# Kernel tuning notes

Measured on AMD Instinct MI355X. Metric: run time of the kernel, lower is better.

## Reference

```python
import jax, jax.numpy as jnp
import numpy as np

# SSMBlock constants (from init_kwargs and standard mamba_ssm defaults)
W = 8            # pooled spatial edge; d_model = W^3
K = 16           # AvgPool3d kernel & stride
D_MODEL = W ** 3            # 512
D_STATE = 16
EXPAND = 2
D_INNER = EXPAND * D_MODEL  # 1024
DT_RANK = D_MODEL // 16     # 32 (ceil(512/16))
D_CONV = 4


def setup_inputs() -> dict:
    key = jax.random.key(0)
    ks = jax.random.split(key, 8)
    s = 0.02
    x = jax.random.normal(ks[0], (1, 64, 128, 128, 128), dtype=jnp.float32)
    in_proj_w = jax.random.normal(ks[1], (2 * D_INNER, D_MODEL), jnp.float32) * s
    conv_w = jax.random.normal(ks[2], (D_INNER, D_CONV), jnp.float32) * s
    conv_b = jnp.zeros((D_INNER,), jnp.float32)
    x_proj_w = jax.random.normal(ks[3], (DT_RANK + 2 * D_STATE, D_INNER), jnp.float32) * s
    dt_proj_w = jax.random.normal(ks[4], (D_INNER, DT_RANK), jnp.float32) * s
    dt_proj_b = jax.random.uniform(ks[5], (D_INNER,), jnp.float32, minval=-4.0, maxval=-2.0)
    A_log = jnp.log(jnp.broadcast_to(jnp.arange(1, D_STATE + 1, dtype=jnp.float32), (D_INNER, D_STATE)))
    D = jnp.ones((D_INNER,), jnp.float32)
    out_proj_w = jax.random.normal(ks[6], (D_MODEL, D_INNER), jnp.float32) * s
    return dict(x=x, in_proj_w=in_proj_w, conv_w=conv_w, conv_b=conv_b,
                x_proj_w=x_proj_w, dt_proj_w=dt_proj_w, dt_proj_b=dt_proj_b,
                A_log=A_log, D=D, out_proj_w=out_proj_w)


def _forward(x, in_proj_w, conv_w, conv_b, x_proj_w, dt_proj_w, dt_proj_b, A_log, D, out_proj_w):
    B, C = x.shape[0], x.shape[1]
    # AvgPool3d(K, stride=K): non-overlapping -> reshape + mean
    xp = x.reshape(B, C, W, K, W, K, W, K).mean(axis=(3, 5, 7))  # (B,C,W,W,W)
    seq = xp.reshape(B, C, D_MODEL)  # Mamba input: L = C, d_model = W^3

    # in_proj -> (x, z)
    xz = jnp.einsum('bld,ed->ble', seq, in_proj_w)  # (B,L,2*D_INNER)
    xs, z = jnp.split(xz, 2, axis=-1)

    # causal depthwise conv1d along L + SiLU
    xt = jnp.pad(xs, ((0, 0), (D_CONV - 1, 0), (0, 0))).transpose(0, 2, 1)  # (B,E,L+pad)
    conv = jax.lax.conv_general_dilated(
        xt, conv_w[:, None, :], window_strides=(1,), padding='VALID',
        dimension_numbers=('NCH', 'OIH', 'NCH'), feature_group_count=D_INNER)
    xs = jax.nn.silu(conv.transpose(0, 2, 1) + conv_b)  # (B,L,E)

    # input-dependent dt, B, C
    x_dbl = jnp.einsum('ble,fe->blf', xs, x_proj_w)
    dt, Bs, Cs = jnp.split(x_dbl, [DT_RANK, DT_RANK + D_STATE], axis=-1)
    dt = jax.nn.softplus(jnp.einsum('blr,er->ble', dt, dt_proj_w) + dt_proj_b)  # (B,L,E)

    # selective scan: h_t = exp(dt*A) h_{t-1} + (dt*x) B_t ; y_t = <h_t, C_t> + D*x_t
    A = -jnp.exp(A_log)                                  # (E,S)
    dA = jnp.exp(dt[..., None] * A)                      # (B,L,E,S)
    dBx = (dt * xs)[..., None] * Bs[:, :, None, :]       # (B,L,E,S)

    def step(h, inp):
        da, dbx, c = inp
        h = da * h + dbx                                 # (B,E,S)
        y = jnp.einsum('bes,bs->be', h, c)
        return h, y

    h0 = jnp.zeros((B, D_INNER, D_STATE), xs.dtype)
    _, ys = jax.lax.scan(step, h0, (dA.transpose(1, 0, 2, 3), dBx.transpose(1, 0, 2, 3), Cs.transpose(1, 0, 2)))
    y = ys.transpose(1, 0, 2) + xs * D                   # (B,L,E)

    y = y * jax.nn.silu(z)
    out = jnp.einsum('ble,de->bld', y, out_proj_w)       # (B,L,d_model)
    return out.reshape(B, C, W, W, W)


def reference(x, in_proj_w, conv_w, conv_b, x_proj_w, dt_proj_w, dt_proj_b, A_log, D, out_proj_w):
    return _forward(x, in_proj_w, conv_w, conv_b, x_proj_w, dt_proj_w, dt_proj_b, A_log, D, out_proj_w)
```

## Files before the change

### kernel.cpp

```cpp
#include <hip/hip_runtime.h>
#include <math.h>

typedef float f32x4 __attribute__((ext_vector_type(4)));

__device__ __forceinline__ float dot4v(f32x4 a, f32x4 b){
    return a.x*b.x + a.y*b.y + a.z*b.z + a.w*b.w;
}
__device__ __forceinline__ float dot4(float4 a, float4 b){
    return a.x*b.x + a.y*b.y + a.z*b.z + a.w*b.w;
}

__device__ __forceinline__ float reduce4(float a0, float a1, float a2, float a3, int lane){
    int b0 = lane & 1, b1 = lane & 2;
    float r  = b0 ? a1 : a0;
    float rt = b0 ? a0 : a1;
    r += __shfl_xor(rt, 1);
    float s  = b0 ? a3 : a2;
    float st = b0 ? a2 : a3;
    s += __shfl_xor(st, 1);
    float u  = b1 ? s : r;
    float ut = b1 ? r : s;
    u += __shfl_xor(ut, 2);
    u += __shfl_xor(u, 4);
    u += __shfl_xor(u, 8);
    u += __shfl_xor(u, 16);
    u += __shfl_xor(u, 32);
    return u;
}

__global__ __launch_bounds__(256) void pool_k(const float* __restrict__ x,
                                              float* __restrict__ seq){
    __shared__ float red[4][8];
    int tid  = threadIdx.x;
    int lane = tid & 63;
    int part = tid >> 6;
    int cdh  = blockIdx.x;
    int c  = cdh >> 6;
    int od = (cdh >> 3) & 7;
    int oh = cdh & 7;
    int half = lane >> 5;
    int f    = lane & 31;

    const f32x4* px = (const f32x4*)x;
    size_t base = ((size_t)(c * 128 + od * 16) * 128 + (size_t)(oh * 16 + half)) * 32 + f
                + (size_t)part * 4 * 4096;

    float acc = 0.f;
    #pragma unroll
    for (int ii = 0; ii < 4; ii++){
        size_t o = base + (size_t)ii * 4096;
        #pragma unroll
        for (int jj = 0; jj < 8; jj++){
            f32x4 v = __builtin_nontemporal_load(&px[o + (size_t)jj * 64]);
            acc += (v.x + v.y) + (v.z + v.w);
        }
    }
    acc += __shfl_xor(acc, 1);
    acc += __shfl_xor(acc, 2);
    acc += __shfl_xor(acc, 32);
    if (lane < 32 && (lane & 3) == 0) red[part][lane >> 2] = acc;
    __syncthreads();
    if (tid < 8){
        float v = red[0][tid] + red[1][tid] + red[2][tid] + red[3][tid];
        seq[c * 512 + od * 64 + oh * 8 + tid] = v * (1.0f / 4096.0f);
    }
}

__global__ __launch_bounds__(256) void inproj_k(const float* __restrict__ seq,
                                                const float* __restrict__ Win,
                                                float* __restrict__ xz){
    int lane = threadIdx.x & 63;
    int wid  = blockIdx.x * 4 + (threadIdx.x >> 6);
    int l0 = (wid >> 7) << 3;
    int e0 = (wid & 127) << 4;
    const f32x4* S = (const f32x4*)seq;
    f32x4 sa[8], sb[8];
    #pragma unroll
    for (int r = 0; r < 8; r++){
        sa[r] = S[(size_t)(l0 + r) * 128 + lane];
        sb[r] = S[(size_t)(l0 + r) * 128 + lane + 64];
    }
    #pragma unroll 2
    for (int j = 0; j < 16; j++){
        int e = e0 + j;
        const f32x4* W = (const f32x4*)Win + (size_t)e * 128;
        f32x4 w0 = W[lane], w1 = W[lane + 64];
        float a[8];
        #pragma unroll
        for (int r = 0; r < 8; r++) a[r] = dot4v(w0, sa[r]) + dot4v(w1, sb[r]);
        float u0 = reduce4(a[0], a[1], a[2], a[3], lane);
        float u1 = reduce4(a[4], a[5], a[6], a[7], lane);
        if (lane < 4){
            xz[(size_t)(l0 + lane) * 2048 + e]     = u0;
            xz[(size_t)(l0 + 4 + lane) * 2048 + e] = u1;
        }
    }
}

__global__ __launch_bounds__(256) void xpc_k(const float* __restrict__ xz,
                                             const float* __restrict__ cw,
                                             const float* __restrict__ cb,
                                             const float* __restrict__ Wx,
                                             float* __restrict__ xsT,
                                             float* __restrict__ zsT,
                                             float* __restrict__ bcT,
                                             float* __restrict__ xdT){
    __shared__ float xs_row[1024];
    int bid = blockIdx.x;
    int l  = bid >> 2;
    int fg = bid & 3;
    int t  = threadIdx.x;

    #pragma unroll
    for (int j = 0; j < 4; j++){
        int e = t + j * 256;
        float v = cb[e];
        #pragma unroll
        for (int tt = 0; tt < 4; tt++){
            int ll = l - 3 + tt;
            if (ll >= 0) v += cw[e * 4 + tt] * xz[(size_t)ll * 2048 + e];
        }
        v = v / (1.f + expf(-v));
        xs_row[e] = v;
        if (fg == 0){
            xsT[(size_t)e * 64 + l] = v;
            float zv = xz[(size_t)l * 2048 + 1024 + e];
            zsT[(size_t)e * 64 + l] = zv / (1.f + expf(-zv));
        }
    }
    __syncthreads();

    int f = fg * 16 + (t >> 4);
    int q = t & 15;
    const float4* X  = (const float4*)xs_row;
    const float4* W4 = (const float4*)(Wx + (size_t)f * 1024);
    float acc = 0.f;
    #pragma unroll
    for (int k4 = 0; k4 < 16; k4++){
        int idx = q * 16 + k4;
        acc += dot4(X[idx], W4[idx]);
    }
    acc += __shfl_xor(acc, 1);
    acc += __shfl_xor(acc, 2);
    acc += __shfl_xor(acc, 4);
    acc += __shfl_xor(acc, 8);
    if (q == 0){
        if (f < 32) xdT[(size_t)f * 64 + l] = acc;
        else        bcT[(size_t)(f - 32) * 64 + l] = acc;
    }
}

__global__ __launch_bounds__(256) void scan_k(const float* __restrict__ xdT,
                                              const float* __restrict__ bcT,
                                              const float* __restrict__ xsT,
                                              const float* __restrict__ zsT,
                                              const float* __restrict__ Wdt,
                                              const float* __restrict__ bdt,
                                              const float* __restrict__ A_log,
                                              const float* __restrict__ Dv,
                                              float* __restrict__ y){
    __shared__ float red[4][64];
    int e    = blockIdx.x;
    int lane = threadIdx.x & 63;
    int w    = threadIdx.x >> 6;

    float acc = bdt[e];
    #pragma unroll 8
    for (int k = 0; k < 32; k++) acc += xdT[k * 64 + lane] * Wdt[e * 32 + k];
    float dtv = (acc > 20.f) ? acc : log1pf(expf(acc));
    float xv  = xsT[(size_t)e * 64 + lane];

    float py = 0.f;
    #pragma unroll
    for (int i = 0; i < 4; i++){
        int s = w * 4 + i;
        float A = -expf(A_log[e * 16 + s]);
        float a = expf(dtv * A);
        float b = (dtv * xv) * bcT[s * 64 + lane];
        #pragma unroll
        for (int d = 1; d < 64; d <<= 1){
            float ap = __shfl_up(a, d);
            float bp = __shfl_up(b, d);
            if (lane >= d){ b += a * bp; a *= ap; }
        }
        py += b * bcT[(16 + s) * 64 + lane];
    }
    red[w][lane] = py;
    __syncthreads();
    if (threadIdx.x < 64){
        float tot = red[0][lane] + red[1][lane] + red[2][lane] + red[3][lane];
        float yv = (tot + xv * Dv[e]) * zsT[(size_t)e * 64 + lane];
        y[(size_t)lane * 1024 + e] = yv;
    }
}

__global__ __launch_bounds__(256) void outproj_k(const float* __restrict__ y,
                                                 const float* __restrict__ Wo,
                                                 float* __restrict__ out){
    int lane = threadIdx.x & 63;
    int wid  = blockIdx.x * 4 + (threadIdx.x >> 6);
    int l0 = (wid >> 5) << 2;
    int d0 = (wid & 31) << 4;
    const float4* Y = (const float4*)y;
    float4 y0[4], y1[4], y2[4], y3[4];
    #pragma unroll
    for (int q = 0; q < 4; q++){
        y0[q] = Y[(size_t)(l0+0)*256 + q*64 + lane];
        y1[q] = Y[(size_t)(l0+1)*256 + q*64 + lane];
        y2[q] = Y[(size_t)(l0+2)*256 + q*64 + lane];
        y3[q] = Y[(size_t)(l0+3)*256 + q*64 + lane];
    }
    #pragma unroll 2
    for (int j = 0; j < 16; j++){
        int d = d0 + j;
        const float4* W = (const float4*)Wo + (size_t)d * 256;
        float a0 = 0.f, a1 = 0.f, a2 = 0.f, a3 = 0.f;
        #pragma unroll
        for (int q = 0; q < 4; q++){
            float4 w = W[q * 64 + lane];
            a0 += dot4(w, y0[q]);
            a1 += dot4(w, y1[q]);
            a2 += dot4(w, y2[q]);
            a3 += dot4(w, y3[q]);
        }
        float u = reduce4(a0, a1, a2, a3, lane);
        if (lane < 4) out[(size_t)(l0 + lane) * 512 + d] = u;
    }
}

extern "C" void kernel_launch(void* const* d_in, const int* in_sizes, int n_in,
                              void* d_out, int out_size, void* d_ws, size_t ws_size,
                              hipStream_t stream){
    const float* x          = (const float*)d_in[0];
    const float* in_proj_w  = (const float*)d_in[1];
    const float* conv_w     = (const float*)d_in[2];
    const float* conv_b     = (const float*)d_in[3];
    const float* x_proj_w   = (const float*)d_in[4];
    const float* dt_proj_w  = (const float*)d_in[5];
    const float* dt_proj_b  = (const float*)d_in[6];
    const float* A_log      = (const float*)d_in[7];
    const float* Dv         = (const float*)d_in[8];
    const float* out_proj_w = (const float*)d_in[9];
    float* out = (float*)d_out;

    float* ws   = (float*)d_ws;
    float* seq  = ws;
    float* xz   = ws + 32768;
    float* xsT  = ws + 163840;
    float* zsT  = ws + 229376;
    float* bcT  = ws + 294912;
    float* xdT  = ws + 296960;
    float* y    = ws + 299008;

    hipLaunchKernelGGL(pool_k,    dim3(4096), dim3(256), 0, stream, x, seq);
    hipLaunchKernelGGL(inproj_k,  dim3(256),  dim3(256), 0, stream, seq, in_proj_w, xz);
    hipLaunchKernelGGL(xpc_k,     dim3(256),  dim3(256), 0, stream, xz, conv_w, conv_b,
                       x_proj_w, xsT, zsT, bcT, xdT);
    hipLaunchKernelGGL(scan_k,    dim3(1024), dim3(256), 0, stream, xdT, bcT, xsT, zsT,
                       dt_proj_w, dt_proj_b, A_log, Dv, y);
    hipLaunchKernelGGL(outproj_k, dim3(128),  dim3(256), 0, stream, y, out_proj_w, out);
}
```

Measured before the change: 125.2 us.

## Fuse post-pool stages into one persistent kernel with software grid barriers

Merges the in-projection, conv/x-projection, scan and out-projection kernels into a single 512-block persistent kernel. Stages are separated by a flag-based global barrier, and pool_k zeroes the barrier flags. This removes three kernel launch gaps and lets work be split across more blocks (out-projection now uses 8 rows per wave over 512 waves). It relies on all 512 blocks being co-resident, otherwise the barrier spins until its timeout. The barrier adds atomic polling overhead, and the timeout fallback could let a stage run on incomplete data.

Measured after the change: 332.6 us. 2.66x slower.

```diff
diff --git a/kernel.cpp b/kernel.cpp
--- a/kernel.cpp
+++ b/kernel.cpp
@@ -28,13 +28,51 @@
     return u;
 }
 
+#define NBLK 512
+__device__ __forceinline__ void gbar(unsigned* flags, unsigned* rel, unsigned round){
+    __syncthreads();
+    int tid = threadIdx.x;
+    if (blockIdx.x == 0){
+        if (tid == 0){
+            __threadfence();
+            __hip_atomic_store(&flags[0], round, __ATOMIC_RELEASE, __HIP_MEMORY_SCOPE_AGENT);
+        }
+        unsigned it = 0;
+        while (__hip_atomic_load(&flags[tid], __ATOMIC_ACQUIRE, __HIP_MEMORY_SCOPE_AGENT) < round
+               && ++it < 4000000u){}
+        it = 0;
+        while (__hip_atomic_load(&flags[tid + 256], __ATOMIC_ACQUIRE, __HIP_MEMORY_SCOPE_AGENT) < round
+               && ++it < 4000000u){}
+        __syncthreads();
+        if (tid == 0){
+            __hip_atomic_store(rel, round, __ATOMIC_RELEASE, __HIP_MEMORY_SCOPE_AGENT);
+            __threadfence();
+        }
+        __syncthreads();
+    } else {
+        if (tid == 0){
+            __threadfence();
+            __hip_atomic_store(&flags[blockIdx.x], round, __ATOMIC_RELEASE, __HIP_MEMORY_SCOPE_AGENT);
+            unsigned it = 0;
+            while (__hip_atomic_load(rel, __ATOMIC_ACQUIRE, __HIP_MEMORY_SCOPE_AGENT) < round
+                   && ++it < 4000000u){}
+            __threadfence();
+        }
+        __syncthreads();
+    }
+}
+
 __global__ __launch_bounds__(256) void pool_k(const float* __restrict__ x,
-                                              float* __restrict__ seq){
+                                              float* __restrict__ seq,
+                                              unsigned* __restrict__ bar){
     __shared__ float red[4][8];
     int tid  = threadIdx.x;
     int lane = tid & 63;
     int part = tid >> 6;
     int cdh  = blockIdx.x;
+    if (cdh == 0){
+        for (int i = tid; i < 520; i += 256) bar[i] = 0u;
+    }
     int c  = cdh >> 6;
     int od = (cdh >> 3) & 7;
     int oh = cdh & 7;
@@ -66,165 +104,161 @@
     }
 }
 
-__global__ __launch_bounds__(256) void inproj_k(const float* __restrict__ seq,
-                                                const float* __restrict__ Win,
-                                                float* __restrict__ xz){
-    int lane = threadIdx.x & 63;
-    int wid  = blockIdx.x * 4 + (threadIdx.x >> 6);
-    int l0 = (wid >> 7) << 3;
-    int e0 = (wid & 127) << 4;
-    const f32x4* S = (const f32x4*)seq;
-    f32x4 sa[8], sb[8];
-    #pragma unroll
-    for (int r = 0; r < 8; r++){
-        sa[r] = S[(size_t)(l0 + r) * 128 + lane];
-        sb[r] = S[(size_t)(l0 + r) * 128 + lane + 64];
-    }
-    #pragma unroll 2
-    for (int j = 0; j < 16; j++){
-        int e = e0 + j;
-        const f32x4* W = (const f32x4*)Win + (size_t)e * 128;
-        f32x4 w0 = W[lane], w1 = W[lane + 64];
-        float a[8];
-        #pragma unroll
-        for (int r = 0; r < 8; r++) a[r] = dot4v(w0, sa[r]) + dot4v(w1, sb[r]);
-        float u0 = reduce4(a[0], a[1], a[2], a[3], lane);
-        float u1 = reduce4(a[4], a[5], a[6], a[7], lane);
-        if (lane < 4){
-            xz[(size_t)(l0 + lane) * 2048 + e]     = u0;
-            xz[(size_t)(l0 + 4 + lane) * 2048 + e] = u1;
-        }
-    }
-}
-
-__global__ __launch_bounds__(256) void xpc_k(const float* __restrict__ xz,
-                                             const float* __restrict__ cw,
-                                             const float* __restrict__ cb,
-                                             const float* __restrict__ Wx,
-                                             float* __restrict__ xsT,
-                                             float* __restrict__ zsT,
-                                             float* __restrict__ bcT,
-                                             float* __restrict__ xdT){
-    __shared__ float xs_row[1024];
-    int bid = blockIdx.x;
-    int l  = bid >> 2;
-    int fg = bid & 3;
-    int t  = threadIdx.x;
-
-    #pragma unroll
-    for (int j = 0; j < 4; j++){
-        int e = t + j * 256;
-        float v = cb[e];
-        #pragma unroll
-        for (int tt = 0; tt < 4; tt++){
-            int ll = l - 3 + tt;
-            if (ll >= 0) v += cw[e * 4 + tt] * xz[(size_t)ll * 2048 + e];
-        }
-        v = v / (1.f + expf(-v));
-        xs_row[e] = v;
-        if (fg == 0){
-            xsT[(size_t)e * 64 + l] = v;
-            float zv = xz[(size_t)l * 2048 + 1024 + e];
-            zsT[(size_t)e * 64 + l] = zv / (1.f + expf(-zv));
-        }
-    }
-    __syncthreads();
-
-    int f = fg * 16 + (t >> 4);
-    int q = t & 15;
-    const float4* X  = (const float4*)xs_row;
-    const float4* W4 = (const float4*)(Wx + (size_t)f * 1024);
-    float acc = 0.f;
-    #pragma unroll
-    for (int k4 = 0; k4 < 16; k4++){
-        int idx = q * 16 + k4;
-        acc += dot4(X[idx], W4[idx]);
-    }
-    acc += __shfl_xor(acc, 1);
-    acc += __shfl_xor(acc, 2);
-    acc += __shfl_xor(acc, 4);
-    acc += __shfl_xor(acc, 8);
-    if (q == 0){
-        if (f < 32) xdT[(size_t)f * 64 + l] = acc;
-        else        bcT[(size_t)(f - 32) * 64 + l] = acc;
-    }
-}
-
-__global__ __launch_bounds__(256) void scan_k(const float* __restrict__ xdT,
-                                              const float* __restrict__ bcT,
-                                              const float* __restrict__ xsT,
-                                              const float* __restrict__ zsT,
-                                              const float* __restrict__ Wdt,
-                                              const float* __restrict__ bdt,
-                                              const float* __restrict__ A_log,
-                                              const float* __restrict__ Dv,
-                                              float* __restrict__ y){
-    __shared__ float red[4][64];
-    int e    = blockIdx.x;
-    int lane = threadIdx.x & 63;
-    int w    = threadIdx.x >> 6;
-
-    float acc = bdt[e];
-    #pragma unroll 8
-    for (int k = 0; k < 32; k++) acc += xdT[k * 64 + lane] * Wdt[e * 32 + k];
-    float dtv = (acc > 20.f) ? acc : log1pf(expf(acc));
-    float xv  = xsT[(size_t)e * 64 + lane];
-
-    float py = 0.f;
-    #pragma unroll
-    for (int i = 0; i < 4; i++){
-        int s = w * 4 + i;
-        float A = -expf(A_log[e * 16 + s]);
-        float a = expf(dtv * A);
-        float b = (dtv * xv) * bcT[s * 64 + lane];
-        #pragma unroll
-        for (int d = 1; d < 64; d <<= 1){
-            float ap = __shfl_up(a, d);
-            float bp = __shfl_up(b, d);
-            if (lane >= d){ b += a * bp; a *= ap; }
-        }
-        py += b * bcT[(16 + s) * 64 + lane];
-    }
-    red[w][lane] = py;
-    __syncthreads();
-    if (threadIdx.x < 64){
-        float tot = red[0][lane] + red[1][lane] + red[2][lane] + red[3][lane];
-        float yv = (tot + xv * Dv[e]) * zsT[(size_t)e * 64 + lane];
-        y[(size_t)lane * 1024 + e] = yv;
-    }
-}
-
-__global__ __launch_bounds__(256) void outproj_k(const float* __restrict__ y,
-                                                 const float* __restrict__ Wo,
-                                                 float* __restrict__ out){
-    int lane = threadIdx.x & 63;
-    int wid  = blockIdx.x * 4 + (threadIdx.x >> 6);
-    int l0 = (wid >> 5) << 2;
-    int d0 = (wid & 31) << 4;
-    const float4* Y = (const float4*)y;
-    float4 y0[4], y1[4], y2[4], y3[4];
-    #pragma unroll
-    for (int q = 0; q < 4; q++){
-        y0[q] = Y[(size_t)(l0+0)*256 + q*64 + lane];
-        y1[q] = Y[(size_t)(l0+1)*256 + q*64 + lane];
-        y2[q] = Y[(size_t)(l0+2)*256 + q*64 + lane];
-        y3[q] = Y[(size_t)(l0+3)*256 + q*64 + lane];
-    }
-    #pragma unroll 2
-    for (int j = 0; j < 16; j++){
-        int d = d0 + j;
-        const float4* W = (const float4*)Wo + (size_t)d * 256;
-        float a0 = 0.f, a1 = 0.f, a2 = 0.f, a3 = 0.f;
-        #pragma unroll
-        for (int q = 0; q < 4; q++){
-            float4 w = W[q * 64 + lane];
-            a0 += dot4(w, y0[q]);
-            a1 += dot4(w, y1[q]);
-            a2 += dot4(w, y2[q]);
-            a3 += dot4(w, y3[q]);
-        }
-        float u = reduce4(a0, a1, a2, a3, lane);
-        if (lane < 4) out[(size_t)(l0 + lane) * 512 + d] = u;
+__global__ __launch_bounds__(256, 2) void mega_k(
+        const float* __restrict__ seq,  const float* __restrict__ Win,
+        float* __restrict__ xz,
+        const float* __restrict__ cw,   const float* __restrict__ cb,
+        const float* __restrict__ Wx,
+        float* __restrict__ xsT, float* __restrict__ zsT,
+        float* __restrict__ bcT, float* __restrict__ xdT,
+        const float* __restrict__ Wdt,  const float* __restrict__ bdt,
+        const float* __restrict__ A_log,const float* __restrict__ Dv,
+        float* __restrict__ y,
+        const float* __restrict__ Wo,   float* __restrict__ out,
+        unsigned* __restrict__ bar){
+    __shared__ float sh[1024];
+    unsigned* flags = bar;
+    unsigned* rel   = bar + NBLK;
+    int tid  = threadIdx.x;
+    int lane = tid & 63;
+    int bid  = blockIdx.x;
+    int wid  = bid * 4 + (tid >> 6);
+
+    {
+        int l0 = (wid >> 8) << 3;
+        int e0 = (wid & 255) << 3;
+        const f32x4* S = (const f32x4*)seq;
+        f32x4 sa[8], sb[8];
+        #pragma unroll
+        for (int r = 0; r < 8; r++){
+            sa[r] = S[(size_t)(l0 + r) * 128 + lane];
+            sb[r] = S[(size_t)(l0 + r) * 128 + lane + 64];
+        }
+        #pragma unroll 2
+        for (int j = 0; j < 8; j++){
+            int e = e0 + j;
+            const f32x4* W = (const f32x4*)Win + (size_t)e * 128;
+            f32x4 w0 = W[lane], w1 = W[lane + 64];
+            float a[8];
+            #pragma unroll
+            for (int r = 0; r < 8; r++) a[r] = dot4v(w0, sa[r]) + dot4v(w1, sb[r]);
+            float u0 = reduce4(a[0], a[1], a[2], a[3], lane);
+            float u1 = reduce4(a[4], a[5], a[6], a[7], lane);
+            if (lane < 4){
+                xz[(size_t)(l0 + lane) * 2048 + e]     = u0;
+                xz[(size_t)(l0 + 4 + lane) * 2048 + e] = u1;
+            }
+        }
+    }
+    gbar(flags, rel, 1u);
+
+    if (bid < 256){
+        int l  = bid >> 2;
+        int fg = bid & 3;
+        #pragma unroll
+        for (int j = 0; j < 4; j++){
+            int e = tid + j * 256;
+            float v = cb[e];
+            #pragma unroll
+            for (int tt = 0; tt < 4; tt++){
+                int ll = l - 3 + tt;
+                if (ll >= 0) v += cw[e * 4 + tt] * xz[(size_t)ll * 2048 + e];
+            }
+            v = v / (1.f + expf(-v));
+            sh[e] = v;
+            if (fg == 0){
+                xsT[(size_t)e * 64 + l] = v;
+                float zv = xz[(size_t)l * 2048 + 1024 + e];
+                zsT[(size_t)e * 64 + l] = zv / (1.f + expf(-zv));
+            }
+        }
+        __syncthreads();
+
+        int f = fg * 16 + (tid >> 4);
+        int q = tid & 15;
+        const float4* X  = (const float4*)sh;
+        const float4* W4 = (const float4*)(Wx + (size_t)f * 1024);
+        float acc = 0.f;
+        #pragma unroll
+        for (int k4 = 0; k4 < 16; k4++){
+            int idx = q * 16 + k4;
+            acc += dot4(X[idx], W4[idx]);
+        }
+        acc += __shfl_xor(acc, 1);
+        acc += __shfl_xor(acc, 2);
+        acc += __shfl_xor(acc, 4);
+        acc += __shfl_xor(acc, 8);
+        if (q == 0){
+            if (f < 32) xdT[(size_t)f * 64 + l] = acc;
+            else        bcT[(size_t)(f - 32) * 64 + l] = acc;
+        }
+    }
+    gbar(flags, rel, 2u);
+
+    for (int e = bid; e < 1024; e += NBLK){
+        __syncthreads();
+        int w = tid >> 6;
+
+        float acc = bdt[e];
+        #pragma unroll 8
+        for (int k = 0; k < 32; k++) acc += xdT[k * 64 + lane] * Wdt[e * 32 + k];
+        float dtv = (acc > 20.f) ? acc : log1pf(expf(acc));
+        float xv  = xsT[(size_t)e * 64 + lane];
+
+        float py = 0.f;
+        #pragma unroll
+        for (int i = 0; i < 4; i++){
+            int s = w * 4 + i;
+            float A = -expf(A_log[e * 16 + s]);
+            float a = expf(dtv * A);
+            float b = (dtv * xv) * bcT[s * 64 + lane];
+            #pragma unroll
+            for (int d = 1; d < 64; d <<= 1){
+                float ap = __shfl_up(a, d);
+                float bp = __shfl_up(b, d);
+                if (lane >= d){ b += a * bp; a *= ap; }
+            }
+            py += b * bcT[(16 + s) * 64 + lane];
+        }
+        sh[w * 64 + lane] = py;
+        __syncthreads();
+        if (tid < 64){
+            float tot = sh[lane] + sh[64 + lane] + sh[128 + lane] + sh[192 + lane];
+            float yv = (tot + xv * Dv[e]) * zsT[(size_t)e * 64 + lane];
+            y[(size_t)lane * 1024 + e] = yv;
+        }
+    }
+    gbar(flags, rel, 3u);
+
+    if (wid < 512){
+        int l0 = (wid >> 6) << 3;
+        int d0 = (wid & 63) << 3;
+        const f32x4* Y = (const f32x4*)y;
+        f32x4 yr[8][4];
+        #pragma unroll
+        for (int r = 0; r < 8; r++){
+            #pragma unroll
+            for (int q = 0; q < 4; q++)
+                yr[r][q] = Y[(size_t)(l0 + r) * 256 + q * 64 + lane];
+        }
+        #pragma unroll 2
+        for (int j = 0; j < 8; j++){
+            int d = d0 + j;
+            const f32x4* W = (const f32x4*)Wo + (size_t)d * 256;
+            float a[8] = {0,0,0,0,0,0,0,0};
+            #pragma unroll
+            for (int q = 0; q < 4; q++){
+                f32x4 w = W[q * 64 + lane];
+                #pragma unroll
+                for (int r = 0; r < 8; r++) a[r] += dot4v(w, yr[r][q]);
+            }
+            float u0 = reduce4(a[0], a[1], a[2], a[3], lane);
+            float u1 = reduce4(a[4], a[5], a[6], a[7], lane);
+            if (lane < 4){
+                out[(size_t)(l0 + lane) * 512 + d]     = u0;
+                out[(size_t)(l0 + 4 + lane) * 512 + d] = u1;
+            }
+        }
     }
 }
 
@@ -251,12 +285,11 @@
     float* bcT  = ws + 294912;
     float* xdT  = ws + 296960;
     float* y    = ws + 299008;
-
-    hipLaunchKernelGGL(pool_k,    dim3(4096), dim3(256), 0, stream, x, seq);
-    hipLaunchKernelGGL(inproj_k,  dim3(256),  dim3(256), 0, stream, seq, in_proj_w, xz);
-    hipLaunchKernelGGL(xpc_k,     dim3(256),  dim3(256), 0, stream, xz, conv_w, conv_b,
-                       x_proj_w, xsT, zsT, bcT, xdT);
-    hipLaunchKernelGGL(scan_k,    dim3(1024), dim3(256), 0, stream, xdT, bcT, xsT, zsT,
-                       dt_proj_w, dt_proj_b, A_log, Dv, y);
-    hipLaunchKernelGGL(outproj_k, dim3(128),  dim3(256), 0, stream, y, out_proj_w, out);
-}
+    unsigned* bar = (unsigned*)(ws + 364544);
+
+    hipLaunchKernelGGL(pool_k, dim3(4096), dim3(256), 0, stream, x, seq, bar);
+    hipLaunchKernelGGL(mega_k, dim3(NBLK), dim3(256), 0, stream,
+                       seq, in_proj_w, xz, conv_w, conv_b, x_proj_w,
+                       xsT, zsT, bcT, xdT, dt_proj_w, dt_proj_b, A_log, Dv,
+                       y, out_proj_w, out, bar);
+}
```
